# Performance work log

Hardware: AMD Instinct MI355X
Metric: run time of the kernel (lower is better)

## Reference

```python
import jax, jax.numpy as jnp
import numpy as np

NEG = -jnp.inf


def _pipeline(logits, presence_penalties, frequency_penalties, repetition_penalties,
              temperatures, top_p, min_p, top_a, tfs, typical_p,
              epsilon_cutoff, eta_cutoff, smoothing_factor, smoothing_curve,
              prompt_tokens, output_tokens, top_k):
    N, V = logits.shape
    rows = jnp.arange(N)[:, None]
    cols = jnp.arange(V)[None, :]

    # ---- presence / frequency / repetition penalties (bincount via scatter-add) ----
    pbin = jnp.zeros((N, V + 1), jnp.int32).at[rows, prompt_tokens].add(1)[:, :V]
    obin = jnp.zeros((N, V + 1), jnp.int32).at[rows, output_tokens].add(1)[:, :V]
    seen = (pbin > 0) | (obin > 0)
    rp = jnp.where(seen, repetition_penalties[:, None], 1.0)
    logits = jnp.where(logits > 0, logits / rp, logits * rp)
    logits = logits - frequency_penalties[:, None] * obin.astype(logits.dtype)
    logits = logits - presence_penalties[:, None] * (obin > 0).astype(logits.dtype)

    # ---- temperature ----
    logits = logits / temperatures[:, None]

    # ---- top-k + top-p (sort ascending, mask, unsort) ----
    order = jnp.argsort(logits, axis=-1)               # ascending
    ls = jnp.take_along_axis(logits, order, axis=-1)
    kth_pos = (V - jnp.clip(top_k.astype(jnp.int32), 1, V))[:, None]
    kth_val = jnp.take_along_axis(ls, kth_pos, axis=1)
    ls = jnp.where(ls < kth_val, NEG, ls)
    cs = jnp.cumsum(jax.nn.softmax(ls, axis=-1), axis=-1)
    pmask = (cs <= (1.0 - top_p)[:, None]).at[:, -1].set(False)
    ls = jnp.where(pmask, NEG, ls)
    logits = jnp.take_along_axis(ls, jnp.argsort(order, axis=-1), axis=-1)

    # ---- tail-free sampling (sort descending, 2nd-derivative CDF cutoff) ----
    order_d = jnp.argsort(-logits, axis=-1)            # descending order of logits
    ls = jnp.take_along_axis(logits, order_d, axis=-1)
    probs = jax.nn.softmax(ls, axis=-1)
    d2 = jnp.abs(jnp.diff(jnp.diff(probs, axis=-1), axis=-1))   # (N, V-2)
    cdf = jnp.cumsum(d2 / jnp.sum(d2, axis=-1, keepdims=True), axis=-1)
    m = cdf > tfs[:, None]
    m = jnp.concatenate([jnp.zeros((N, 1), bool), m, jnp.ones((N, 1), bool)], axis=-1)
    ls = jnp.where(m, NEG, ls)
    logits = jnp.take_along_axis(ls, jnp.argsort(order_d, axis=-1), axis=-1)

    # ---- eta cutoff (entropy-adaptive threshold, always keep argmax) ----
    sl = jax.nn.log_softmax(logits, axis=-1)
    probs = jnp.exp(sl)
    sl_safe = jnp.where(probs > 0, sl, 0.0)            # nansum equivalent
    neg_ent = jnp.sum(probs * sl_safe, axis=-1)
    eps = jnp.minimum(eta_cutoff, jnp.sqrt(eta_cutoff) * jnp.exp(neg_ent))[:, None]
    top_idx = jnp.argmax(probs, axis=-1)[:, None]
    logits = jnp.where((probs < eps) & (cols != top_idx), NEG, logits)

    # ---- epsilon cutoff (absolute prob threshold, always keep argmax) ----
    probs = jax.nn.softmax(logits, axis=-1)
    top_idx = jnp.argmax(probs, axis=-1)[:, None]
    logits = jnp.where((probs < epsilon_cutoff[:, None]) & (cols != top_idx), NEG, logits)

    # ---- locally typical sampling ----
    sl = jax.nn.log_softmax(logits, axis=-1)
    probs = jnp.exp(sl)
    sl_safe = jnp.where(probs > 0, sl, 0.0)
    neg_ent = jnp.sum(probs * sl_safe, axis=-1, keepdims=True)
    dev = jnp.abs(neg_ent - sl)                        # surprisal deviation
    order_t = jnp.argsort(dev, axis=-1)
    rp2 = jnp.take_along_axis(probs, order_t, axis=-1)
    msort = (jnp.cumsum(rp2, axis=-1) >= typical_p[:, None]).at[:, 0].set(False)
    mask = jnp.zeros((N, V), bool).at[rows, order_t].set(msort)
    logits = jnp.where(mask, NEG, logits)

    # ---- quadratic (smoothing) sampling ----
    mx = jnp.max(logits, axis=-1, keepdims=True)
    finite = logits != NEG
    diff = jnp.where(finite, logits, mx) - mx          # finite everywhere
    kq = (3.0 - smoothing_curve[:, None]) / 2.0
    sq = (smoothing_curve[:, None] - 1.0) / 2.0
    sfc = smoothing_factor[:, None]
    trans = -(kq * sfc * diff ** 2) + sq * sfc * diff ** 3 + mx
    trans = jnp.where(finite, trans, logits)
    logits = jnp.where(sfc > 0, trans, logits)

    # ---- min-p ----
    probs = jax.nn.softmax(logits, axis=-1)
    top_prob = jnp.max(probs, axis=-1, keepdims=True)
    logits = jnp.where(probs < min_p[:, None] * top_prob, NEG, logits)

    # ---- top-a ----
    probs = jax.nn.softmax(logits, axis=-1)
    top_prob = jnp.max(probs, axis=-1, keepdims=True)
    logits = jnp.where(probs < top_a[:, None] * top_prob ** 2, NEG, logits)

    return logits


def setup_inputs() -> dict:
    N, V, PL, OL = 256, 50257, 512, 128
    ks = jax.random.split(jax.random.key(0), 17)
    u = lambda k, lo, hi: lo + (hi - lo) * jax.random.uniform(k, (N,), jnp.float32)
    return {
        "logits": 3.0 * jax.random.normal(ks[0], (N, V), jnp.float32),
        "prompt_tokens": jax.random.randint(ks[1], (N, PL), 0, V),
        "output_tokens": jax.random.randint(ks[2], (N, OL), 0, V),
        "presence_penalties": u(ks[3], 0.0, 0.5),
        "frequency_penalties": u(ks[4], 0.0, 0.5),
        "repetition_penalties": u(ks[5], 1.0, 1.3),
        "temperatures": u(ks[6], 0.5, 1.5),
        "top_p": u(ks[7], 0.85, 0.99),
        "top_k": jax.random.randint(ks[8], (N,), 1, 2048, dtype=jnp.int32),
        "min_p": u(ks[9], 0.0, 0.05),
        "top_a": u(ks[10], 0.0, 0.1),
        "tfs": u(ks[11], 0.95, 0.999),
        "typical_p": u(ks[12], 0.9, 0.999),
        "epsilon_cutoff": u(ks[13], 1e-5, 1e-4),
        "eta_cutoff": u(ks[14], 1e-5, 1e-4),
        "smoothing_factor": u(ks[15], 0.05, 0.25),
        "smoothing_curve": u(ks[16], 1.0, 2.0),
    }


def reference(logits, prompt_tokens, output_tokens, presence_penalties,
              frequency_penalties, repetition_penalties, temperatures, top_p,
              top_k, min_p, top_a, tfs, typical_p, epsilon_cutoff, eta_cutoff,
              smoothing_factor, smoothing_curve):
    return _pipeline(logits, presence_penalties, frequency_penalties,
                     repetition_penalties, temperatures, top_p, min_p, top_a,
                     tfs, typical_p, epsilon_cutoff, eta_cutoff,
                     smoothing_factor, smoothing_curve,
                     prompt_tokens, output_tokens, top_k)
```

## Files before the change

### kernel.cpp

```cpp
#include <hip/hip_runtime.h>
#include <stdint.h>

#define TPB 1024
#define NWAVE 16
#define MAXK 2304
#define NV4 13
#define BIG_NEG (-1.0e30f)

__device__ __forceinline__ uint32_t fkey(float x) {
  uint32_t s = __float_as_uint(x);
  return (s & 0x80000000u) ? ~s : (s | 0x80000000u);
}
__device__ __forceinline__ float fkey_inv(uint32_t u) {
  uint32_t s = (u & 0x80000000u) ? (u & 0x7fffffffu) : ~u;
  return __uint_as_float(s);
}
__device__ __forceinline__ unsigned long long shfl_xor_u64(unsigned long long v, int m) {
  uint32_t lo = (uint32_t)v, hi = (uint32_t)(v >> 32);
  lo = (uint32_t)__shfl_xor((int)lo, m, 64);
  hi = (uint32_t)__shfl_xor((int)hi, m, 64);
  return (((unsigned long long)hi) << 32) | lo;
}

struct TokMem { uint32_t obin[12568]; uint32_t seen[1600]; };
struct SortMem { unsigned long long kp[4096]; };
union __align__(16) U1 { TokMem tok; SortMem srt; };

__device__ __forceinline__ float block_sum1(float v, float* buf) {
  int lane = threadIdx.x & 63, wd = threadIdx.x >> 6;
#pragma unroll
  for (int off = 32; off > 0; off >>= 1) v += __shfl_down(v, off, 64);
  if (lane == 0) buf[wd] = v;
  __syncthreads();
  const float4* b4 = (const float4*)buf;
  float4 A = b4[0], B = b4[1], C = b4[2], D = b4[3];
  float r = A.x; r += A.y; r += A.z; r += A.w;
  r += B.x; r += B.y; r += B.z; r += B.w;
  r += C.x; r += C.y; r += C.z; r += C.w;
  r += D.x; r += D.y; r += D.z; r += D.w;
  return r;
}

__device__ __forceinline__ float wbuf_prefix(const float* wbuf, int wd) {
  const float4* w4 = (const float4*)wbuf;
  float4 a = w4[0], b = w4[1], c = w4[2], d = w4[3];
  float t[16] = {a.x, a.y, a.z, a.w, b.x, b.y, b.z, b.w,
                 c.x, c.y, c.z, c.w, d.x, d.y, d.z, d.w};
  float base = 0.f;
#pragma unroll
  for (int i = 0; i < 16; ++i) base += (i < wd) ? t[i] : 0.f;
  return base;
}

__device__ __forceinline__ int wave_reduce_int(int v) {
#pragma unroll
  for (int off = 32; off > 0; off >>= 1) v += __shfl_down(v, off, 64);
  return __shfl(v, 0, 64);
}

template <class Pred>
__device__ __forceinline__ int wave_psearch(int lo, int hi, Pred pred) {
  const int lane = (int)threadIdx.x & 63;
  while (lo <= hi) {
    int range = hi - lo + 1;
    int stride = (range + 63) >> 6;
    long long p = (long long)lo + (long long)stride * lane;
    bool q = (p <= hi) ? pred((int)p) : false;
    unsigned long long bm = __ballot(q);
    int h = bm ? (63 - (int)__clzll(bm)) : -1;
    int nlo = (h >= 0) ? (int)((long long)lo + (long long)stride * h + 1) : lo;
    long long pf = (long long)lo + (long long)stride * (h + 1);
    int nhi = (pf <= (long long)hi) ? (int)pf - 1 : hi;
    if (nlo > nhi) return nlo;
    lo = nlo; hi = nhi;
  }
  return lo;
}

__device__ void block_scan3x3(const float* __restrict__ se, float* __restrict__ sp,
                              float* __restrict__ sq, float* __restrict__ sr, int m,
                              float* wA, float* wB, float* wC) {
  int tid = (int)threadIdx.x, lane = tid & 63, wd = tid >> 6;
  int b = tid * 3;
  __syncthreads();
  float e0 = (b     < m) ? se[b]     : 0.f;
  float e1 = (b + 1 < m) ? se[b + 1] : 0.f;
  float e2 = (b + 2 < m) ? se[b + 2] : 0.f;
  float e3 = (b + 3 < m) ? se[b + 3] : 0.f;
  float e4 = (b + 4 < m) ? se[b + 4] : 0.f;
  float q0 = (b     < m) ? sq[b]     : 0.f;
  float q1 = (b + 1 < m) ? sq[b + 1] : 0.f;
  float q2 = (b + 2 < m) ? sq[b + 2] : 0.f;
  float z0 = fabsf((e2 - e1) - (e1 - e0));
  float z1 = fabsf((e3 - e2) - (e2 - e1));
  float z2 = fabsf((e4 - e3) - (e3 - e2));
  float ae1 = e0 + e1, ae2 = ae1 + e2;
  float aq1 = q0 + q1, aq2 = aq1 + q2;
  float az1 = z0 + z1, az2 = az1 + z2;
  float tE = ae2, wE = ae2, tQ = aq2, wQ = aq2, tZ = az2, wZ = az2;
#pragma unroll
  for (int off = 1; off < 64; off <<= 1) {
    float sE = __shfl_up(wE, off, 64);
    float sQ = __shfl_up(wQ, off, 64);
    float sZ = __shfl_up(wZ, off, 64);
    if (lane >= off) { wE += sE; wQ += sQ; wZ += sZ; }
  }
  if (lane == 63) { wA[wd] = wE; wB[wd] = wQ; wC[wd] = wZ; }
  __syncthreads();
  float bE = wbuf_prefix(wA, wd), bQ = wbuf_prefix(wB, wd), bZ = wbuf_prefix(wC, wd);
  float xE = bE + (wE - tE), xQ = bQ + (wQ - tQ), xZ = bZ + (wZ - tZ);
  if (b < m)     { sp[b]     = e0 + xE;  sq[b]     = q0 + xQ;  sr[b]     = z0 + xZ; }
  if (b + 1 < m) { sp[b + 1] = ae1 + xE; sq[b + 1] = aq1 + xQ; sr[b + 1] = az1 + xZ; }
  if (b + 2 < m) { sp[b + 2] = ae2 + xE; sq[b + 2] = aq2 + xQ; sr[b + 2] = az2 + xZ; }
  __syncthreads();
}

__device__ uint32_t wave_select_digit2k(const uint32_t* __restrict__ h, uint32_t* w_io) {
  int lane = threadIdx.x & 63;
  uint32_t w = *w_io;
  const int base = lane << 5;
  uint32_t lsum = 0;
#pragma unroll
  for (int t = 0; t < 8; ++t) {
    const int tt = (t + lane) & 7;
    const uint4 v = *(const uint4*)(h + base + tt * 4);
    lsum += v.x + v.y + v.z + v.w;
  }
  uint32_t W = lsum;
#pragma unroll
  for (int off = 1; off < 64; off <<= 1) {
    uint32_t x = (uint32_t)__shfl_down((int)W, off, 64);
    if (lane + off < 64) W += x;
  }
  uint32_t Wn = (uint32_t)__shfl_down((int)W, 1, 64);
  if (lane == 63) Wn = 0;
  const bool isb = (W >= w) && (Wn < w);
  int dloc = -1; uint32_t wloc = 0;
  if (isb) {
    uint32_t sfx = Wn;
#pragma unroll
    for (int t = 31; t >= 0; --t) {
      uint32_t c = h[base + t];
      uint32_t si = sfx + c;
      if (si >= w && sfx < w) { dloc = base + t; wloc = w - sfx; }
      sfx = si;
    }
  }
  unsigned long long bm = __ballot(dloc >= 0);
  int src = (int)__popcll(bm - 1ull);
  uint32_t d = (uint32_t)__shfl(dloc, src, 64);
  *w_io = (uint32_t)__shfl((int)wloc, src, 64);
  return d;
}

__device__ uint32_t wave_select_digit256(const uint32_t* __restrict__ h, uint32_t* w_io) {
  int lane = threadIdx.x & 63;
  uint32_t w = *w_io;
  const uint4 v = ((const uint4*)h)[lane];
  uint32_t c0 = v.x, c1 = v.y, c2 = v.z, c3 = v.w;
  uint32_t t0 = c0 + c1 + c2 + c3;
  uint32_t W = t0;
#pragma unroll
  for (int off = 1; off < 64; off <<= 1) {
    uint32_t x = (uint32_t)__shfl_down((int)W, off, 64);
    if (lane + off < 64) W += x;
  }
  uint32_t Wn = (uint32_t)__shfl_down((int)W, 1, 64);
  if (lane == 63) Wn = 0;
  uint32_t S0 = W, S1 = W - c0, S2 = S1 - c1, S3 = S2 - c2, S4 = Wn;
  int dloc = -1; uint32_t wloc = 0;
  if (S0 >= w && S1 < w) { dloc = 4 * lane + 0; wloc = w - S1; }
  if (S1 >= w && S2 < w) { dloc = 4 * lane + 1; wloc = w - S2; }
  if (S2 >= w && S3 < w) { dloc = 4 * lane + 2; wloc = w - S3; }
  if (S3 >= w && S4 < w) { dloc = 4 * lane + 3; wloc = w - S4; }
  unsigned long long bm = __ballot(dloc >= 0);
  int src = (int)__popcll(bm - 1ull);
  uint32_t d = (uint32_t)__shfl(dloc, src, 64);
  *w_io = (uint32_t)__shfl((int)wloc, src, 64);
  return d;
}

template <int NE, bool PING>
__device__ void hybrid_sort(unsigned long long* kp, unsigned long long* kb1, int n) {
  const int tid = (int)threadIdx.x;
  unsigned long long k[NE];
#pragma unroll
  for (int e = 0; e < NE; ++e) {
    int i = e * TPB + tid;
    k[e] = (i < n) ? kp[i] : ~0ull;
  }
  int pb = 0;
  for (int kk = 2; kk <= n; kk <<= 1) {
    for (int j = kk >> 1; j > 0; j >>= 1) {
      if (j >= TPB) {
        const int em = j / TPB;
#pragma unroll
        for (int e = 0; e < NE; ++e) {
          if ((e & em) == 0 && (e + em) < NE) {
            int e2 = e + em;
            int i = e * TPB + tid;
            bool up = ((i & kk) == 0);
            if ((k[e] > k[e2]) == up) {
              unsigned long long tk = k[e]; k[e] = k[e2]; k[e2] = tk;
            }
          }
        }
      } else if (j >= 64) {
        unsigned long long* kb = (PING && pb) ? kb1 : kp;
#pragma unroll
        for (int e = 0; e < NE; ++e) {
          int i = e * TPB + tid;
          if (i < n) kb[i] = k[e];
        }
        __syncthreads();
#pragma unroll
        for (int e = 0; e < NE; ++e) {
          int i = e * TPB + tid;
          if (i < n) {
            unsigned long long o = kb[i ^ j];
            bool up = ((i & kk) == 0);
            bool lower = ((i & j) == 0);
            bool takeMin = (lower == up);
            bool takeOther = takeMin ? (o < k[e]) : (o > k[e]);
            if (takeOther) k[e] = o;
          }
        }
        if (PING) pb ^= 1;
        else __syncthreads();
      } else {
#pragma unroll
        for (int e = 0; e < NE; ++e) {
          int i = e * TPB + tid;
          unsigned long long o = shfl_xor_u64(k[e], j);
          bool up = ((i & kk) == 0);
          bool lower = ((i & j) == 0);
          bool takeMin = (lower == up);
          bool takeOther = takeMin ? (o < k[e]) : (o > k[e]);
          if (takeOther) k[e] = o;
        }
      }
    }
  }
  __syncthreads();
#pragma unroll
  for (int e = 0; e < NE; ++e) {
    int i = e * TPB + tid;
    if (i < n) kp[i] = k[e];
  }
  __syncthreads();
}

__device__ __forceinline__ uint32_t penal_val(float l, int j, bool sn,
    const uint32_t* __restrict__ obin,
    float f_rep, float inv_rep, float f_freq, float f_pres, float inv_temp) {
  int ob = 0;
  if (sn) ob = (int)((obin[j >> 2] >> (8 * (j & 3))) & 255u);
  l = (l > 0.0f) ? (l * (sn ? inv_rep : 1.0f)) : (l * (sn ? f_rep : 1.0f));
  l = l - f_freq * (float)ob;
  l = l - ((ob > 0) ? f_pres : 0.0f);
  l = l * inv_temp;
  return fkey(l);
}

#define FOR_ELEMS(...) do {                                                   \
    if (tid < head) { int j = tid; uint32_t u = uh; (void)j; (void)u; __VA_ARGS__; } \
    _Pragma("unroll")                                                         \
    for (int s4_ = 0; s4_ < NV4; ++s4_) {                                     \
      int iv_ = s4_ * TPB + tid;                                              \
      if (iv_ < nvec) {                                                       \
        int jb_ = head + 4 * iv_;                                             \
        { int j = jb_ + 0; uint32_t u = uk[s4_ * 4 + 0]; (void)j; (void)u; __VA_ARGS__; } \
        { int j = jb_ + 1; uint32_t u = uk[s4_ * 4 + 1]; (void)j; (void)u; __VA_ARGS__; } \
        { int j = jb_ + 2; uint32_t u = uk[s4_ * 4 + 2]; (void)j; (void)u; __VA_ARGS__; } \
        { int j = jb_ + 3; uint32_t u = uk[s4_ * 4 + 3]; (void)j; (void)u; __VA_ARGS__; } \
      }                                                                       \
    }                                                                         \
    if (tid < ntail) { int j = head + 4 * nvec + tid; uint32_t u = ut; (void)j; (void)u; __VA_ARGS__; } \
  } while (0)

__global__ __launch_bounds__(TPB, 4)
void sampler_kernel(const float* __restrict__ logits,
                    const int* __restrict__ ptoks, const int* __restrict__ otoks,
                    const float* __restrict__ pres, const float* __restrict__ freq,
                    const float* __restrict__ rep, const float* __restrict__ temp,
                    const float* __restrict__ topp, const int* __restrict__ topk,
                    const float* __restrict__ minp, const float* __restrict__ topa,
                    const float* __restrict__ tfsv, const float* __restrict__ typp,
                    const float* __restrict__ epsc, const float* __restrict__ etac,
                    const float* __restrict__ smf, const float* __restrict__ smc,
                    float* __restrict__ out, int N, int V, int PL, int OL) {
  __shared__ U1 u1;
  __shared__ __align__(16) uint32_t s_hist2k[2048];
  __shared__ __align__(16) uint32_t s_h256[256];
  __shared__ float s_e[MAXK];
  __shared__ float s_p[MAXK];
  __shared__ float s_q[MAXK];
  __shared__ float s_r[MAXK];
  __shared__ unsigned long long kb1[2048];
  __shared__ __align__(16) float s_site[12][NWAVE];
  __shared__ uint32_t s_cnt;
  __shared__ int s_K, s_ilo, s_ihi;

  const int tid = (int)threadIdx.x;
  const int r = (int)blockIdx.x;
  const int wd = tid >> 6;
  const int lane = tid & 63;

  const float* lrow = logits + (size_t)r * V;
  float* orow = out + (size_t)r * V;

  uintptr_t ra = (uintptr_t)lrow;
  int head = (int)(((16u - (uint32_t)(ra & 15u)) & 15u) >> 2);
  if (head > V) head = V;
  const int nvec = (V - head) >> 2;
  const int ntail = V - head - (nvec << 2);

  float4 lv[NV4];
  float lh = 0.f, lt = 0.f;
#pragma unroll
  for (int s4 = 0; s4 < NV4; ++s4) {
    int iv = s4 * TPB + tid;
    if (iv < nvec) lv[s4] = *(const float4*)(lrow + head + 4 * iv);
  }
  if (tid < head) lh = lrow[tid];
  if (tid < ntail) lt = lrow[head + 4 * nvec + tid];
  int pt = -1, ot = -1;
  if (tid < PL) pt = ptoks[(size_t)r * PL + tid];
  if (tid < OL) ot = otoks[(size_t)r * OL + tid];

  const float f_pres = pres[r], f_freq = freq[r], f_rep = rep[r], f_temp = temp[r];
  const float f_topp = topp[r], f_minp = minp[r], f_topa = topa[r], f_tfs = tfsv[r];
  const float f_typp = typp[r], f_epsc = epsc[r], f_etac = etac[r];
  const float f_smf = smf[r], f_smc = smc[r];
  const float inv_rep = 1.0f / f_rep, inv_temp = 1.0f / f_temp;
  int k_topk = topk[r];
  if (k_topk < 1) k_topk = 1;
  if (k_topk > V) k_topk = V;

  {
    const uint4 z4 = make_uint4(0u, 0u, 0u, 0u);
    uint4* ob4 = (uint4*)u1.tok.obin;
    for (int i = tid; i < 3142; i += TPB) ob4[i] = z4;
    uint4* se4 = (uint4*)u1.tok.seen;
    for (int i = tid; i < 400; i += TPB) se4[i] = z4;
    uint4* h4 = (uint4*)s_hist2k;
    for (int i = tid; i < 512; i += TPB) h4[i] = z4;
    if (tid < 64) ((uint4*)s_h256)[tid] = z4;
  }
  if (tid == 0) s_cnt = 0;
  __syncthreads();
  if ((unsigned)pt < (unsigned)V) atomicOr(&u1.tok.seen[pt >> 5], 1u << (pt & 31));
  for (int i = TPB + tid; i < PL; i += TPB) {
    int t = ptoks[(size_t)r * PL + i];
    if ((unsigned)t < (unsigned)V) atomicOr(&u1.tok.seen[t >> 5], 1u << (t & 31));
  }
  if ((unsigned)ot < (unsigned)V) {
    atomicOr(&u1.tok.seen[ot >> 5], 1u << (ot & 31));
    atomicAdd(&u1.tok.obin[ot >> 2], 1u << (8 * (ot & 3)));
  }
  for (int i = TPB + tid; i < OL; i += TPB) {
    int t = otoks[(size_t)r * OL + i];
    if ((unsigned)t < (unsigned)V) {
      atomicOr(&u1.tok.seen[t >> 5], 1u << (t & 31));
      atomicAdd(&u1.tok.obin[t >> 2], 1u << (8 * (t & 3)));
    }
  }
  __syncthreads();

  const uint32_t* seenp = u1.tok.seen;
  const uint32_t* obinp = u1.tok.obin;

  uint32_t uk[NV4 * 4];
  uint32_t uh = 0, ut = 0;
#pragma unroll
  for (int s4 = 0; s4 < NV4; ++s4) {
    int iv = s4 * TPB + tid;
    uint32_t u0 = 0, u1k = 0, u2k = 0, u3 = 0;
    if (iv < nvec) {
      const float4 lvv = lv[s4];
      int jb = head + 4 * iv;
      uint32_t w0 = seenp[jb >> 5];
      uint32_t w1 = seenp[(jb >> 5) + 1];
      uint32_t sb = (uint32_t)(((((uint64_t)w1) << 32) | (uint64_t)w0) >> (jb & 31));
      u0 = penal_val(lvv.x, jb + 0, (sb >> 0) & 1u, obinp, f_rep, inv_rep, f_freq, f_pres, inv_temp);
      u1k = penal_val(lvv.y, jb + 1, (sb >> 1) & 1u, obinp, f_rep, inv_rep, f_freq, f_pres, inv_temp);
      u2k = penal_val(lvv.z, jb + 2, (sb >> 2) & 1u, obinp, f_rep, inv_rep, f_freq, f_pres, inv_temp);
      u3 = penal_val(lvv.w, jb + 3, (sb >> 3) & 1u, obinp, f_rep, inv_rep, f_freq, f_pres, inv_temp);
      atomicAdd(&s_hist2k[u0 >> 21], 1u);
      atomicAdd(&s_hist2k[u1k >> 21], 1u);
      atomicAdd(&s_hist2k[u2k >> 21], 1u);
      atomicAdd(&s_hist2k[u3 >> 21], 1u);
    }
    uk[s4 * 4 + 0] = u0; uk[s4 * 4 + 1] = u1k; uk[s4 * 4 + 2] = u2k; uk[s4 * 4 + 3] = u3;
  }
  {
    bool snh = false, snt = false;
    if (tid < head) snh = (seenp[tid >> 5] >> (tid & 31)) & 1u;
    if (tid < head)
      uh = penal_val(lh, tid, snh, obinp, f_rep, inv_rep, f_freq, f_pres, inv_temp);
    if (tid < head) atomicAdd(&s_hist2k[uh >> 21], 1u);
    int jt = head + 4 * nvec + tid;
    if (tid < ntail) snt = (seenp[jt >> 5] >> (jt & 31)) & 1u;
    if (tid < ntail)
      ut = penal_val(lt, jt, snt, obinp, f_rep, inv_rep, f_freq, f_pres, inv_temp);
    if (tid < ntail) atomicAdd(&s_hist2k[ut >> 21], 1u);
  }

  {
    uintptr_t oa = (uintptr_t)orow;
    int ohead = (int)(((16u - (uint32_t)(oa & 15u)) & 15u) >> 2);
    if (ohead > V) ohead = V;
    int onvec = (V - ohead) >> 2;
    for (int j = tid; j < ohead; j += TPB) orow[j] = BIG_NEG;
    float4* o4 = (float4*)(orow + ohead);
    const float4 f4 = make_float4(BIG_NEG, BIG_NEG, BIG_NEG, BIG_NEG);
    for (int i = tid; i < onvec; i += TPB) o4[i] = f4;
    for (int j = ohead + (onvec << 2) + tid; j < V; j += TPB) orow[j] = BIG_NEG;
  }
  __syncthreads();

  uint32_t w = (uint32_t)k_topk;
  uint32_t d11 = wave_select_digit2k(s_hist2k, &w);
  FOR_ELEMS(if ((u >> 21) == d11) atomicAdd(&s_h256[(u >> 13) & 255u], 1u));
  __syncthreads();
  uint32_t d8 = wave_select_digit256(s_h256, &w);
  const uint32_t kth_u = (d11 << 21) | (d8 << 13);

  unsigned long long* kp = u1.srt.kp;
  {
    int cnt_t = 0;
    FOR_ELEMS(cnt_t += (u >= kth_u) ? 1 : 0);
    int incl = cnt_t;
#pragma unroll
    for (int off = 1; off < 64; off <<= 1) {
      int x = __shfl_up(incl, off, 64);
      if (lane >= off) incl += x;
    }
    int wtot = __shfl(incl, 63, 64);
    uint32_t base = 0;
    if (lane == 0 && wtot > 0) base = atomicAdd(&s_cnt, (uint32_t)wtot);
    base = (uint32_t)__shfl((int)base, 0, 64);
    uint32_t off_t = base + (uint32_t)(incl - cnt_t);
    FOR_ELEMS(
      if (u >= kth_u) {
        if (off_t < MAXK)
          kp[off_t] = (((unsigned long long)(~u)) << 16) | (unsigned long long)(uint32_t)j;
        off_t++;
      });
  }
  __syncthreads();
  int K = (int)s_cnt;
  if (K > MAXK) K = MAXK;

  {
    int n1 = 64; while (n1 < K) n1 <<= 1;
    for (int i = K + tid; i < n1; i += TPB) kp[i] = ~0ull;
    __syncthreads();
    if (n1 <= 1024) hybrid_sort<1, true>(kp, kb1, n1);
    else if (n1 == 2048) hybrid_sort<2, true>(kp, kb1, n1);
    else hybrid_sort<4, false>(kp, nullptr, n1);
  }

  if (wd == 0) {
    const uint32_t kth_inv = (uint32_t)(kp[k_topk - 1] >> 16);
    int KT = wave_psearch(0, K - 1, [&](int i) {
      return (uint32_t)(kp[i] >> 16) <= kth_inv;
    });
    if (lane == 0) s_K = KT;
  }
  __syncthreads();
  K = s_K;

  const float m0 = fkey_inv(~(uint32_t)(kp[0] >> 16));

  for (int i = tid; i < K; i += TPB) {
    float v = fkey_inv(~(uint32_t)(kp[i] >> 16));
    float e = __expf(v - m0);
    s_e[i] = e; s_q[i] = e * (v - m0);
  }
  block_scan3x3(s_e, s_p, s_q, s_r, K, s_site[7], s_site[8], s_site[9]);

  int i_lo = 0, i_hi = K - 1;
  if (wd == 0) {
    const float S = s_p[K - 1];

    const float thS = (1.0f - f_topp) * S;
    int cnt = 0;
    for (int i = lane; i < K; i += 64) {
      float ss = S - s_p[i] + s_e[i];
      if (i == 0 || ss > thS) cnt++;
    }
    int K1 = wave_reduce_int(cnt);

    auto dzAt = [&](int i, int mm) -> float {
      float x0 = s_e[i];
      float x1 = (i + 1 < mm) ? s_e[i + 1] : 0.f;
      float x2 = (i + 2 < mm) ? s_e[i + 2] : 0.f;
      return fabsf((x2 - x1) - (x1 - x0));
    };
    int K2;
    if (K1 >= 2) {
      float base = (K1 >= 3) ? s_r[K1 - 3] : 0.f;
      float rKm2 = base + dzAt(K1 - 2, K1);
      float rKm1 = rKm2 + dzAt(K1 - 1, K1);
      const float thT = f_tfs * rKm1;
      const int Km3 = K1 - 3;
      K2 = 1 + wave_psearch(0, K1 - 2, [&](int j) {
        float rj = (j <= Km3) ? s_r[j] : rKm2;
        return rj <= thT;
      });
    } else K2 = 1;

    const float SD = s_p[K2 - 1];
    const float neD = s_q[K2 - 1] / SD - __logf(SD);
    const float eps = fminf(f_etac, sqrtf(f_etac) * __expf(neD));
    const float thD = eps * SD;
    int K3 = wave_psearch(1, K2 - 1, [&](int i) { return s_e[i] >= thD; });

    const float thE = f_epsc * s_p[K3 - 1];
    int K4 = wave_psearch(1, K3 - 1, [&](int i) { return s_e[i] >= thE; });

    const float SF = s_p[K4 - 1];
    const float lseF = __logf(SF);
    const float neF = s_q[K4 - 1] / SF - lseF;
    const float vth = neF + lseF + m0;
    const float typSF = f_typp * SF;
    const int c = wave_psearch(0, K4 - 1, [&](int i) {
      return fkey_inv(~(uint32_t)(kp[i] >> 16)) >= vth;
    });
    const int nB = K4 - c;

    auto keyAt = [&](int i) -> unsigned long long {
      unsigned long long kk = kp[i];
      float v = fkey_inv(~(uint32_t)(kk >> 16));
      return (((unsigned long long)fkey(fabsf(v - vth))) << 16) | (kk & 0xffffull);
    };
    auto splitFor = [&](int p) -> int {
      int alo = p - nB; if (alo < 0) alo = 0;
      int ahi = (p < c) ? p : c;
      while (alo < ahi) {
        int am = (alo + ahi + 1) >> 1;
        int tb = p - am;
        bool take = true;
        if (tb < nB) take = (keyAt(c - am) <= keyAt(c + tb));
        if (take) alo = am; else ahi = am - 1;
      }
      return alo;
    };
    auto massLess = [&](int p) -> bool {
      int a = splitFor(p);
      int b = p - a;
      float sum = s_p[c + b - 1] - ((c - a > 0) ? s_p[c - a - 1] : 0.f);
      return sum < typSF;
    };
    int plo = 0, phi = K4;
    while (phi > plo) {
      int range = phi - plo;
      int stride = (range + 63) >> 6;
      int p = plo + stride * (lane + 1);
      bool q = false;
      if (p <= phi) q = massLess(p);
      unsigned long long bm = __ballot(q);
      int h = bm ? (63 - (int)__clzll(bm)) : -1;
      int nlo = (h >= 0) ? (plo + stride * (h + 1)) : plo;
      long long nf = (long long)plo + (long long)stride * (long long)(h + 2);
      int nhi = (nf <= (long long)phi) ? (int)nf - 1 : phi;
      plo = nlo; phi = nhi;
    }
    int L = plo;
    if (L < 1) L = 1;
    if (L > K4) L = K4;
    int a = splitFor(L);
    if (lane == 0) { s_ilo = c - a; s_ihi = c + (L - a) - 1; }
  }
  __syncthreads();
  i_lo = s_ilo; i_hi = s_ihi;

  float S2;
  const float mx = fkey_inv(~(uint32_t)(kp[i_lo] >> 16));
  {
    const float kq = (3.0f - f_smc) * 0.5f;
    const float sq = (f_smc - 1.0f) * 0.5f;
    float pS = 0.f;
    for (int i = i_lo + tid; i <= i_hi; i += TPB) {
      float v = fkey_inv(~(uint32_t)(kp[i] >> 16));
      float d = v - mx;
      float tr = mx - (kq * f_smf) * (d * d) + (sq * f_smf) * ((d * d) * d);
      float v2 = (f_smf > 0.0f) ? tr : v;
      float e = __expf(v2 - mx);
      s_q[i] = e;
      s_r[i] = v2;
      if (e >= f_minp) pS += e;
    }
    S2 = block_sum1(pS, s_site[6]);
  }

  {
    const float thA = f_topa / S2;
    for (int i = i_lo + tid; i <= i_hi; i += TPB) {
      float e = s_q[i];
      if (e >= f_minp && e >= thA) {
        int idx = (int)(kp[i] & 0xffffull);
        orow[idx] = s_r[i];
      }
    }
  }
}

extern "C" void kernel_launch(void* const* d_in, const int* in_sizes, int n_in,
                              void* d_out, int out_size, void* d_ws, size_t ws_size,
                              hipStream_t stream) {
  const float* logits = (const float*)d_in[0];
  const int* ptoks = (const int*)d_in[1];
  const int* otoks = (const int*)d_in[2];
  const float* pres = (const float*)d_in[3];
  const float* freq = (const float*)d_in[4];
  const float* rep  = (const float*)d_in[5];
  const float* temp = (const float*)d_in[6];
  const float* topp = (const float*)d_in[7];
  const int*   topk = (const int*)d_in[8];
  const float* minp = (const float*)d_in[9];
  const float* topa = (const float*)d_in[10];
  const float* tfsv = (const float*)d_in[11];
  const float* typp = (const float*)d_in[12];
  const float* epsc = (const float*)d_in[13];
  const float* etac = (const float*)d_in[14];
  const float* smf  = (const float*)d_in[15];
  const float* smc  = (const float*)d_in[16];

  int N = in_sizes[3];
  int V = in_sizes[0] / N;
  int PL = in_sizes[1] / N;
  int OL = in_sizes[2] / N;

  sampler_kernel<<<N, TPB, 0, stream>>>(logits, ptoks, otoks, pres, freq, rep, temp,
                                        topp, topk, minp, topa, tfsv, typp, epsc, etac,
                                        smf, smc, (float*)d_out, N, V, PL, OL);
}
```

Before: 70.75 us.

## Fuse candidate compaction into second-digit histogram pass with staged boundary bucket

The second radix-select histogram pass now also writes elements whose top digit exceeds the selected digit straight into the candidate buffer. It stages the elements in the boundary digit bucket into a scratch array using wave ballot compaction. After the second digit is picked, only the staged bucket is filtered, not a rescan of the whole row with a count-and-scan. This removes one full register pass over the row and the per-thread prefix scan. In exchange it adds a ballot and an atomic per unrolled element in the histogram pass, and falls back to a full rescan if the boundary bucket overflows 2048 entries.

```diff
diff --git a/kernel.cpp b/kernel.cpp
--- a/kernel.cpp
+++ b/kernel.cpp
@@ -276,6 +276,36 @@
       }                                                                       \
     }                                                                         \
     if (tid < ntail) { int j = head + 4 * nvec + tid; uint32_t u = ut; (void)j; (void)u; __VA_ARGS__; } \
+  } while (0)
+
+#define PUSH_KP(pred_) do {                                                   \
+    bool pk_ = (pred_);                                                       \
+    unsigned long long bm_ = __ballot(pk_);                                   \
+    if (bm_) {                                                                \
+      uint32_t base_ = 0;                                                     \
+      if (lane == 0) base_ = atomicAdd(&s_cnt, (uint32_t)__popcll(bm_));      \
+      base_ = (uint32_t)__shfl((int)base_, 0, 64);                            \
+      if (pk_) {                                                              \
+        uint32_t pos_ = base_ + (uint32_t)__popcll(bm_ & ((1ull << (unsigned)lane) - 1ull)); \
+        if (pos_ < MAXK)                                                      \
+          kp[pos_] = (((unsigned long long)(~u)) << 16) | (unsigned long long)(uint32_t)j; \
+      }                                                                       \
+    }                                                                         \
+  } while (0)
+
+#define STAGE_KB(pred_) do {                                                  \
+    bool pk_ = (pred_);                                                       \
+    unsigned long long bm_ = __ballot(pk_);                                   \
+    if (bm_) {                                                                \
+      uint32_t base_ = 0;                                                     \
+      if (lane == 0) base_ = atomicAdd(&s_cnt2, (uint32_t)__popcll(bm_));     \
+      base_ = (uint32_t)__shfl((int)base_, 0, 64);                            \
+      if (pk_) {                                                              \
+        uint32_t pos_ = base_ + (uint32_t)__popcll(bm_ & ((1ull << (unsigned)lane) - 1ull)); \
+        if (pos_ < 2048)                                                      \
+          kb1[pos_] = (((unsigned long long)(~u)) << 16) | (unsigned long long)(uint32_t)j; \
+      }                                                                       \
+    }                                                                         \
   } while (0)
 
 __global__ __launch_bounds__(TPB, 4)
@@ -298,7 +328,7 @@
   __shared__ float s_r[MAXK];
   __shared__ unsigned long long kb1[2048];
   __shared__ __align__(16) float s_site[12][NWAVE];
-  __shared__ uint32_t s_cnt;
+  __shared__ uint32_t s_cnt, s_cnt2;
   __shared__ int s_K, s_ilo, s_ihi;
 
   const int tid = (int)threadIdx.x;
@@ -347,7 +377,7 @@
     for (int i = tid; i < 512; i += TPB) h4[i] = z4;
     if (tid < 64) ((uint4*)s_h256)[tid] = z4;
   }
-  if (tid == 0) s_cnt = 0;
+  if (tid == 0) { s_cnt = 0; s_cnt2 = 0; }
   __syncthreads();
   if ((unsigned)pt < (unsigned)V) atomicOr(&u1.tok.seen[pt >> 5], 1u << (pt & 31));
   for (int i = TPB + tid; i < PL; i += TPB) {
@@ -421,32 +451,40 @@
 
   uint32_t w = (uint32_t)k_topk;
   uint32_t d11 = wave_select_digit2k(s_hist2k, &w);
-  FOR_ELEMS(if ((u >> 21) == d11) atomicAdd(&s_h256[(u >> 13) & 255u], 1u));
-  __syncthreads();
+
+  unsigned long long* kp = u1.srt.kp;
+  FOR_ELEMS({
+    uint32_t dig = u >> 21;
+    bool eq = (dig == d11);
+    if (eq) atomicAdd(&s_h256[(u >> 13) & 255u], 1u);
+    PUSH_KP(dig > d11);
+    STAGE_KB(eq);
+  });
+  __syncthreads();
+
   uint32_t d8 = wave_select_digit256(s_h256, &w);
   const uint32_t kth_u = (d11 << 21) | (d8 << 13);
-
-  unsigned long long* kp = u1.srt.kp;
   {
-    int cnt_t = 0;
-    FOR_ELEMS(cnt_t += (u >= kth_u) ? 1 : 0);
-    int incl = cnt_t;
-#pragma unroll
-    for (int off = 1; off < 64; off <<= 1) {
-      int x = __shfl_up(incl, off, 64);
-      if (lane >= off) incl += x;
-    }
-    int wtot = __shfl(incl, 63, 64);
-    uint32_t base = 0;
-    if (lane == 0 && wtot > 0) base = atomicAdd(&s_cnt, (uint32_t)wtot);
-    base = (uint32_t)__shfl((int)base, 0, 64);
-    uint32_t off_t = base + (uint32_t)(incl - cnt_t);
-    FOR_ELEMS(
-      if (u >= kth_u) {
-        if (off_t < MAXK)
-          kp[off_t] = (((unsigned long long)(~u)) << 16) | (unsigned long long)(uint32_t)j;
-        off_t++;
-      });
+    const uint32_t inv_fl = ~kth_u;
+    uint32_t nst = s_cnt2;
+    if (nst <= 2048u) {
+      for (uint32_t i = (uint32_t)tid; i < nst; i += TPB) {
+        unsigned long long pk64 = kb1[i];
+        bool keep = ((uint32_t)(pk64 >> 16) <= inv_fl);
+        unsigned long long bm_ = __ballot(keep);
+        if (bm_) {
+          uint32_t base_ = 0;
+          if (lane == 0) base_ = atomicAdd(&s_cnt, (uint32_t)__popcll(bm_));
+          base_ = (uint32_t)__shfl((int)base_, 0, 64);
+          if (keep) {
+            uint32_t pos_ = base_ + (uint32_t)__popcll(bm_ & ((1ull << (unsigned)lane) - 1ull));
+            if (pos_ < MAXK) kp[pos_] = pk64;
+          }
+        }
+      }
+    } else {
+      FOR_ELEMS(PUSH_KP(((u >> 21) == d11) && (u >= kth_u)));
+    }
   }
   __syncthreads();
   int K = (int)s_cnt;
```

Measured after the change: 83.32 us. 17.8% more time.
